# Performance work log

Measured on AMD Instinct MI355X. Metric: run time of the kernel, lower is better.

Reference implementation:

```python
import jax, jax.numpy as jnp
import numpy as np

N, E = 50000, 800000
IN, HID, OUT = 128, 32, 8


def setup_inputs() -> dict:
    key = jax.random.key(0)
    ks = jax.random.split(key, 20)
    f32 = jnp.float32
    def rn(k, shape, s=0.1):
        return (jax.random.normal(k, shape, dtype=f32) * s)
    return {
        'x': jax.random.normal(ks[0], (N, IN), dtype=f32),
        'edge_index': jax.random.randint(ks[1], (2, E), 0, N, dtype=jnp.int32),
        'edge_attr': jax.random.uniform(ks[2], (E, 1), dtype=f32),
        # layer 1: heads=4, out=HID, concat -> 4*HID channels
        'w1l': rn(ks[3], (IN, 4 * HID)), 'b1l': rn(ks[4], (4 * HID,)),
        'w1r': rn(ks[5], (IN, 4 * HID)), 'b1r': rn(ks[6], (4 * HID,)),
        'w1e': rn(ks[7], (1, 4 * HID)),
        'att1': rn(ks[8], (4, HID)), 'bias1': rn(ks[9], (4 * HID,)),
        # layer 2: heads=2, out=HID, mean over heads -> HID channels
        'w2l': rn(ks[10], (4 * HID, 2 * HID)), 'b2l': rn(ks[11], (2 * HID,)),
        'w2r': rn(ks[12], (4 * HID, 2 * HID)), 'b2r': rn(ks[13], (2 * HID,)),
        'w2e': rn(ks[14], (1, 2 * HID)),
        'att2': rn(ks[15], (2, HID)), 'bias2': rn(ks[16], (HID,)),
        'wc': rn(ks[17], (HID, OUT)), 'bc': rn(ks[18], (OUT,)),
    }


def _add_self_loops(edge_index, edge_attr, n):
    # PyG GATv2Conv adds self-loops; edge feature for loops = mean of edge_attr
    loop = jnp.arange(n, dtype=edge_index.dtype)
    src = jnp.concatenate([edge_index[0], loop])
    dst = jnp.concatenate([edge_index[1], loop])
    mean_attr = jnp.broadcast_to(edge_attr.mean(axis=0), (n, edge_attr.shape[1]))
    ea = jnp.concatenate([edge_attr, mean_attr], axis=0)
    return src, dst, ea


def _gatv2(x, src, dst, eattr, Wl, bl, Wr, br, We, att, bias, heads, out, concat):
    n = x.shape[0]
    xl = (x @ Wl + bl).reshape(n, heads, out)   # source transform (messages)
    xr = (x @ Wr + br).reshape(n, heads, out)   # target transform
    e = (eattr @ We).reshape(-1, heads, out)    # edge embedding
    z = jax.nn.leaky_relu(xl[src] + xr[dst] + e, negative_slope=0.2)  # [Etot,H,D]
    score = jnp.einsum('ehd,hd->eh', z, att)
    # segment softmax over incoming edges of each destination node
    smax = jax.ops.segment_max(score, dst, num_segments=n)
    ex = jnp.exp(score - smax[dst])
    denom = jax.ops.segment_sum(ex, dst, num_segments=n)
    alpha = ex / denom[dst]                     # [Etot,H]
    agg = jax.ops.segment_sum(xl[src] * alpha[..., None], dst, num_segments=n)
    o = agg.reshape(n, heads * out) if concat else agg.mean(axis=1)
    return o + bias


def reference(x, edge_index, edge_attr, w1l, b1l, w1r, b1r, w1e, att1, bias1,
              w2l, b2l, w2r, b2r, w2e, att2, bias2, wc, bc):
    src, dst, ea = _add_self_loops(edge_index, edge_attr, x.shape[0])
    h = _gatv2(x, src, dst, ea, w1l, b1l, w1r, b1r, w1e, att1, bias1, 4, HID, True)
    h = jax.nn.elu(h)
    # dropout p=0.4 is training-only; reference is eval mode (identity)
    h = _gatv2(h, src, dst, ea, w2l, b2l, w2r, b2r, w2e, att2, bias2, 2, HID, False)
    h = jax.nn.elu(h)
    return h @ wc + bc
```

## Files before the change

### kernel.cpp

```cpp
#include <hip/hip_runtime.h>
#include <hip/hip_fp16.h>
#include <math.h>

typedef _Float16 h2_t __attribute__((ext_vector_type(2)));
typedef _Float16 h4_t __attribute__((ext_vector_type(4)));
typedef _Float16 h8_t __attribute__((ext_vector_type(8)));
typedef float f4_t __attribute__((ext_vector_type(4)));
typedef float f8_t __attribute__((ext_vector_type(8)));

#define PRE_BLOCKS 512
#define SB 512
#define NBUK_PAD 800

__device__ inline h8_t load8f_to_h8(const float* p) {
    float4 a = *(const float4*)p;
    float4 b = *(const float4*)(p + 4);
    h8_t r;
    r[0] = (_Float16)a.x; r[1] = (_Float16)a.y; r[2] = (_Float16)a.z; r[3] = (_Float16)a.w;
    r[4] = (_Float16)b.x; r[5] = (_Float16)b.y; r[6] = (_Float16)b.z; r[7] = (_Float16)b.w;
    return r;
}

__device__ inline h4_t load4f_to_h4(const float* p) {
    float4 a = *(const float4*)p;
    h4_t r;
    r[0] = (_Float16)a.x; r[1] = (_Float16)a.y; r[2] = (_Float16)a.z; r[3] = (_Float16)a.w;
    return r;
}

__device__ inline float dot8h(h8_t a, h8_t b, float s) {
    s = __builtin_amdgcn_fdot2(__builtin_shufflevector(a, a, 0, 1),
                               __builtin_shufflevector(b, b, 0, 1), s, false);
    s = __builtin_amdgcn_fdot2(__builtin_shufflevector(a, a, 2, 3),
                               __builtin_shufflevector(b, b, 2, 3), s, false);
    s = __builtin_amdgcn_fdot2(__builtin_shufflevector(a, a, 4, 5),
                               __builtin_shufflevector(b, b, 4, 5), s, false);
    s = __builtin_amdgcn_fdot2(__builtin_shufflevector(a, a, 6, 7),
                               __builtin_shufflevector(b, b, 6, 7), s, false);
    return s;
}

__device__ inline float dot4h(h4_t a, h4_t b, float s) {
    s = __builtin_amdgcn_fdot2(__builtin_shufflevector(a, a, 0, 1),
                               __builtin_shufflevector(b, b, 0, 1), s, false);
    s = __builtin_amdgcn_fdot2(__builtin_shufflevector(a, a, 2, 3),
                               __builtin_shufflevector(b, b, 2, 3), s, false);
    return s;
}

__device__ inline float elu1(float v) { return v > 0.f ? v : __expf(v) - 1.f; }

struct MA {
    const float* x;
    const float* eattr;
    const int* ei;
    const float *w1l, *b1l, *w1r, *b1r, *w1e, *att1, *bias1;
    const float *w2l, *b2l, *w2r, *b2r, *w2e, *att2, *bias2;
    const float *wc, *bc;
    float* out;
    _Float16 *xh, *xl1h, *xr1h, *h1h, *xl2h, *xr2h;
    _Float16 *p1l, *p1r, *p2l, *p2r;
    int *deg, *offb;
    unsigned* parth;
    unsigned *tstart, *tot;
    unsigned* smeanq;
    unsigned* tmp;
    float* part;
    unsigned* edges;
    int N, E, NW, NBK, CE;
    float invE;
};


__device__ inline void phase_packw(const MA& a, int g) {
    const float* W;
    _Float16* P;
    int M, lg;
    if (g < 2048)      { W = a.w1l; P = a.p1l; M = 128; lg = g; }
    else if (g < 4096) { W = a.w1r; P = a.p1r; M = 128; lg = g - 2048; }
    else if (g < 5120) { W = a.w2l; P = a.p2l; M = 64;  lg = g - 4096; }
    else               { W = a.w2r; P = a.p2r; M = 64;  lg = g - 5120; }
    int ln = lg & 63;
    int s = (lg >> 6) & 3;
    int tt = lg >> 8;
    int m = ln & 15, quad = ln >> 4;
    h8_t v;
#pragma unroll
    for (int j = 0; j < 8; ++j)
        v[j] = (_Float16)W[(size_t)(s * 32 + quad * 8 + j) * M + tt * 16 + m];
    *(h8_t*)(P + (size_t)lg * 8) = v;
}

template <int NT>
__device__ inline void phase_mm_tile(const MA& a, const _Float16* X, int rt, int lane,
                                     const _Float16* Pl, const float* bl, _Float16* Yl,
                                     const _Float16* Pr, const float* br, _Float16* Yr) {
    int nrow = lane & 15, quad = lane >> 4;
    int row = rt * 16 + nrow;
    if (row >= a.N) return;
    const _Float16* xp = X + (size_t)row * 128 + quad * 8;
    h8_t bf0 = *(const h8_t*)(xp);
    h8_t bf1 = *(const h8_t*)(xp + 32);
    h8_t bf2 = *(const h8_t*)(xp + 64);
    h8_t bf3 = *(const h8_t*)(xp + 96);
#pragma unroll
    for (int w = 0; w < 2; ++w) {
        const _Float16* P = w ? Pr : Pl;
        const float* bias = w ? br : bl;
        _Float16* Y = w ? Yr : Yl;
#pragma unroll
        for (int t2 = 0; t2 < NT; ++t2) {
            f4_t acc = {0.f, 0.f, 0.f, 0.f};
            const _Float16* pb = P + (size_t)t2 * 2048 + (size_t)lane * 8;
            acc = __builtin_amdgcn_mfma_f32_16x16x32_f16(*(const h8_t*)pb, bf0, acc, 0, 0, 0);
            acc = __builtin_amdgcn_mfma_f32_16x16x32_f16(*(const h8_t*)(pb + 512), bf1, acc, 0, 0, 0);
            acc = __builtin_amdgcn_mfma_f32_16x16x32_f16(*(const h8_t*)(pb + 1024), bf2, acc, 0, 0, 0);
            acc = __builtin_amdgcn_mfma_f32_16x16x32_f16(*(const h8_t*)(pb + 1536), bf3, acc, 0, 0, 0);
            float4 bv = *(const float4*)(bias + t2 * 16 + quad * 4);
            h4_t o;
            o[0] = (_Float16)(acc[0] + bv.x);
            o[1] = (_Float16)(acc[1] + bv.y);
            o[2] = (_Float16)(acc[2] + bv.z);
            o[3] = (_Float16)(acc[3] + bv.w);
            *(h4_t*)(Y + (size_t)row * (NT * 16) + t2 * 16 + quad * 4) = o;
        }
    }
}


__global__ __launch_bounds__(256) void k_pre(MA a) {
    if (blockIdx.x >= PRE_BLOCKS) {
        int g = (blockIdx.x - PRE_BLOCKS) * 256 + threadIdx.x;
        if (g < 6144) phase_packw(a, g);
        return;
    }
    __shared__ unsigned bh[NBUK_PAD];
    __shared__ float sd[4];
    int tx = threadIdx.x;
    for (int j = tx; j < NBUK_PAD; j += 256) bh[j] = 0u;

    int t = blockIdx.x * 256 + tx;
    const int stride = PRE_BLOCKS * 256;
    int nchunk = (a.N * 128) >> 3;
    for (int i = t; i < nchunk; i += stride) {
        h8_t v = load8f_to_h8(a.x + (size_t)i * 8);
        *(h8_t*)(a.xh + (size_t)i * 8) = v;
    }
    float s = 0.f;
    for (int i = t; i < a.E; i += stride) s += a.eattr[i];
    for (int o = 1; o < 64; o <<= 1) s += __shfl_xor(s, o, 64);
    if ((tx & 63) == 0) sd[tx >> 6] = s;
    __syncthreads();
    if (tx == 0) a.part[blockIdx.x] = sd[0] + sd[1] + sd[2] + sd[3];

    int e0 = blockIdx.x * a.CE, e1 = min(e0 + a.CE, a.E);
    for (int e = e0 + tx; e < e1; e += 256)
        atomicAdd(&bh[((unsigned)a.ei[a.E + e]) >> 6], 1u);
    __syncthreads();
    for (int j = tx; j < NBUK_PAD; j += 256)
        a.parth[(size_t)blockIdx.x * NBUK_PAD + j] = bh[j];
}


__global__ __launch_bounds__(512, 1) void k_colscan(MA a) {
    __shared__ unsigned lds[512];
    int tx = threadIdx.x;
    int b = blockIdx.x;
    unsigned v = a.parth[(size_t)tx * NBUK_PAD + b];
    lds[tx] = v;
    __syncthreads();
    for (int o = 1; o < 512; o <<= 1) {
        unsigned u = (tx >= o) ? lds[tx - o] : 0u;
        __syncthreads();
        lds[tx] += u;
        __syncthreads();
    }
    a.parth[(size_t)tx * NBUK_PAD + b] = lds[tx] - v;
    if (tx == 511) a.tot[b] = lds[511];
}


__global__ __launch_bounds__(1024, 1) void k_scan2(MA a) {
    __shared__ unsigned lds[1024];
    __shared__ float sd[16];
    int tx = threadIdx.x;
    unsigned v = (tx < a.NBK) ? a.tot[tx] : 0u;
    lds[tx] = v;
    float s = (tx < PRE_BLOCKS) ? a.part[tx] : 0.f;
    for (int o = 1; o < 64; o <<= 1) s += __shfl_xor(s, o, 64);
    if ((tx & 63) == 0) sd[tx >> 6] = s;
    __syncthreads();
    for (int o = 1; o < 1024; o <<= 1) {
        unsigned u = (tx >= o) ? lds[tx - o] : 0u;
        __syncthreads();
        lds[tx] += u;
        __syncthreads();
    }
    if (tx < a.NBK) a.tstart[tx] = lds[tx] - v;
    if (tx == 0) {
        float m = 0.f;
#pragma unroll
        for (int k = 0; k < 16; ++k) m += sd[k];
        a.smeanq[0] = (unsigned)__float2int_rn(m * a.invE * 255.f);
    }
}


__global__ __launch_bounds__(256) void k_scatter(MA a) {
    int bid = blockIdx.x;
    if (bid < a.NW) {
        int wid = bid * 4 + (threadIdx.x >> 6);
        int ntile = (a.N + 15) / 16;
        if (wid < ntile)
            phase_mm_tile<8>(a, a.xh, wid, threadIdx.x & 63,
                             a.p1l, a.b1l, a.xl1h, a.p1r, a.b1r, a.xr1h);
        return;
    }
    __shared__ unsigned cur[NBUK_PAD];
    int s = bid - a.NW;
    int tx = threadIdx.x;
    for (int j = tx; j < NBUK_PAD; j += 256)
        cur[j] = a.parth[(size_t)s * NBUK_PAD + j] + a.tstart[j];
    __syncthreads();
    int e0 = s * a.CE, e1 = min(e0 + a.CE, a.E);
    for (int e = e0 + tx; e < e1; e += 256) {
        int d = a.ei[a.E + e];
        unsigned src = (unsigned)a.ei[e];
        unsigned q = (unsigned)__float2int_rn(a.eattr[e] * 255.f);
        unsigned pos = atomicAdd(&cur[d >> 6], 1u);
        a.tmp[pos] = src | (q << 16) | ((unsigned)(d & 63) << 24);
    }
}


__global__ __launch_bounds__(256) void k_fine(MA a) {
    __shared__ int hist[64];
    __shared__ unsigned cur[64];
    __shared__ unsigned sm;
    int b = blockIdx.x;
    int tx = threadIdx.x;
    int n0 = b << 6;
    int nn = min(64, a.N - n0);
    unsigned ts = a.tstart[b], T = a.tot[b];
    if (tx < 64) hist[tx] = 0;
    if (tx == 0) sm = a.smeanq[0];
    __syncthreads();
    for (unsigned i = tx; i < T; i += 256) {
        unsigned v = a.tmp[ts + i];
        atomicAdd(&hist[(int)(v >> 24)], 1);
    }
    __syncthreads();
    if (tx < 64) {
        int deg1 = hist[tx] + 1;
        int vsc = deg1;
#pragma unroll
        for (int o = 1; o < 64; o <<= 1) {
            int u = __shfl_up(vsc, o, 64);
            if (tx >= o) vsc += u;
        }
        int off = (int)ts + n0 + (vsc - deg1);
        if (tx < nn) {
            a.offb[n0 + tx] = off;
            a.deg[n0 + tx] = deg1;
            a.edges[off] = (unsigned)(n0 + tx) | (sm << 24);
        }
        cur[tx] = (unsigned)(off + 1);
    }
    __syncthreads();
    for (unsigned i = tx; i < T; i += 256) {
        unsigned v = a.tmp[ts + i];
        int loc = (int)(v >> 24);
        unsigned pos = atomicAdd(&cur[loc], 1u);
        a.edges[pos] = (v & 0xFFFFu) | (((v >> 16) & 0xFFu) << 24);
    }
}


__global__ __launch_bounds__(256) void k_node1(MA a) {
    int tid = threadIdx.x;
    int q = tid & 15;
    int node = blockIdx.x * 16 + (tid >> 4);
    if (node >= a.N) return;
    unsigned cb = (unsigned)(q * 16);

    h8_t xrv = *(const h8_t*)((const char*)a.xr1h + ((unsigned)node << 8) + cb);
    h8_t wev = load8f_to_h8(a.w1e + q * 8);
    h8_t atv = load8f_to_h8(a.att1 + q * 8);
    const unsigned* ep = a.edges + a.offb[node];
    int deg1 = a.deg[node];
    int last = deg1 - 1;
    const char* xb = (const char*)a.xl1h;

    float l = 0.f;
    f8_t acc = {0.f, 0.f, 0.f, 0.f, 0.f, 0.f, 0.f, 0.f};

    auto GA = [&](unsigned p) -> h8_t {
        return *(const h8_t*)(xb + (((p & 0x00FFFFFFu) << 8) | cb));
    };
    auto LOADG = [&](int i, unsigned& p0, unsigned& p1, unsigned& p2, unsigned& p3,
                     h8_t& x0, h8_t& x1, h8_t& x2, h8_t& x3) {
        p0 = ep[i];
        p1 = ep[min(i + 1, last)];
        p2 = ep[min(i + 2, last)];
        p3 = ep[min(i + 3, last)];
        x0 = GA(p0); x1 = GA(p1); x2 = GA(p2); x3 = GA(p3);
    };
    auto COMPG = [&](int i, unsigned p0, unsigned p1, unsigned p2, unsigned p3,
                     h8_t x0, h8_t x1, h8_t x2, h8_t x3) {
        float e0 = (float)(p0 >> 24) * (1.f / 255.f);
        float e1 = (float)(p1 >> 24) * (1.f / 255.f);
        float e2 = (float)(p2 >> 24) * (1.f / 255.f);
        float e3 = (float)(p3 >> 24) * (1.f / 255.f);
        h8_t z0 = x0 + xrv + wev * (_Float16)e0;
        z0 = __builtin_elementwise_max(z0, z0 * (_Float16)0.2f);
        float sc0 = dot8h(z0, atv, 0.f);
        h8_t z1 = x1 + xrv + wev * (_Float16)e1;
        z1 = __builtin_elementwise_max(z1, z1 * (_Float16)0.2f);
        float sc1 = dot8h(z1, atv, 0.f);
        h8_t z2 = x2 + xrv + wev * (_Float16)e2;
        z2 = __builtin_elementwise_max(z2, z2 * (_Float16)0.2f);
        float sc2 = dot8h(z2, atv, 0.f);
        h8_t z3 = x3 + xrv + wev * (_Float16)e3;
        z3 = __builtin_elementwise_max(z3, z3 * (_Float16)0.2f);
        float sc3 = dot8h(z3, atv, 0.f);
        sc0 += __shfl_xor(sc0, 1, 64); sc0 += __shfl_xor(sc0, 2, 64);
        sc1 += __shfl_xor(sc1, 1, 64); sc1 += __shfl_xor(sc1, 2, 64);
        sc2 += __shfl_xor(sc2, 1, 64); sc2 += __shfl_xor(sc2, 2, 64);
        sc3 += __shfl_xor(sc3, 1, 64); sc3 += __shfl_xor(sc3, 2, 64);
        float pA = __expf(fminf(sc0, 60.f));
        float pB = (i + 1 < deg1) ? __expf(fminf(sc1, 60.f)) : 0.f;
        float pC = (i + 2 < deg1) ? __expf(fminf(sc2, 60.f)) : 0.f;
        float pD = (i + 3 < deg1) ? __expf(fminf(sc3, 60.f)) : 0.f;
        l += (pA + pB) + (pC + pD);
#pragma unroll
        for (int k = 0; k < 8; ++k)
            acc[k] = fmaf(pA, (float)x0[k],
                     fmaf(pB, (float)x1[k],
                     fmaf(pC, (float)x2[k], fmaf(pD, (float)x3[k], acc[k]))));
    };

    unsigned pa0, pa1, pa2, pa3, pb0, pb1, pb2, pb3;
    h8_t xa0, xa1, xa2, xa3, xb0, xb1, xb2, xb3;
    LOADG(0, pa0, pa1, pa2, pa3, xa0, xa1, xa2, xa3);
    for (int i = 0; i < deg1; i += 8) {
        if (i + 4 < deg1) LOADG(i + 4, pb0, pb1, pb2, pb3, xb0, xb1, xb2, xb3);
        COMPG(i, pa0, pa1, pa2, pa3, xa0, xa1, xa2, xa3);
        if (i + 8 < deg1) LOADG(i + 8, pa0, pa1, pa2, pa3, xa0, xa1, xa2, xa3);
        if (i + 4 < deg1) COMPG(i + 4, pb0, pb1, pb2, pb3, xb0, xb1, xb2, xb3);
    }

    float inv = 1.f / l;
    float4 b0 = *(const float4*)(a.bias1 + q * 8);
    float4 b1 = *(const float4*)(a.bias1 + q * 8 + 4);
    float bb[8] = {b0.x, b0.y, b0.z, b0.w, b1.x, b1.y, b1.z, b1.w};
    h8_t o;
#pragma unroll
    for (int k = 0; k < 8; ++k) o[k] = (_Float16)elu1(fmaf(acc[k], inv, bb[k]));
    *(h8_t*)((char*)a.h1h + ((unsigned)node << 8) + cb) = o;
}


__global__ __launch_bounds__(256) void k_mm4(MA a) {
    int wid = blockIdx.x * 4 + (threadIdx.x >> 6);
    int ntile = (a.N + 15) / 16;
    if (wid >= ntile) return;
    phase_mm_tile<4>(a, a.h1h, wid, threadIdx.x & 63,
                     a.p2l, a.b2l, a.xl2h, a.p2r, a.b2r, a.xr2h);
}


__global__ __launch_bounds__(256) void k_node2(MA a) {
    __shared__ float h2s[16][33];
    int tid = threadIdx.x;
    int lane = tid & 63;
    int wib = tid >> 6;
    int sub = lane >> 4;
    int r = lane & 15;
    int nloc = wib * 4 + sub;
    int node = blockIdx.x * 16 + nloc;
    int c0 = r * 4;

    if (node < a.N) {
        h4_t xrv = *(const h4_t*)(a.xr2h + (size_t)node * 64 + c0);
        h4_t wev = load4f_to_h4(a.w2e + c0);
        h4_t atv = load4f_to_h4(a.att2 + c0);
        const unsigned* ep = a.edges + a.offb[node];
        int deg1 = a.deg[node];
        int last = deg1 - 1;
        const char* xb = (const char*)a.xl2h;
        unsigned cb = (unsigned)(c0 * 2);
        float l = 0.f;
        float acc[4] = {0.f, 0.f, 0.f, 0.f};
        for (int i = 0; i < deg1; i += 4) {
            unsigned p[4];
            h4_t xv[4];
#pragma unroll
            for (int j = 0; j < 4; ++j) p[j] = ep[min(i + j, last)];
#pragma unroll
            for (int j = 0; j < 4; ++j)
                xv[j] = *(const h4_t*)(xb + (((p[j] & 0x00FFFFFFu) << 7) | cb));
#pragma unroll
            for (int j = 0; j < 4; ++j) {
                float ea = (float)(p[j] >> 24) * (1.f / 255.f);
                h4_t z = xv[j] + xrv + wev * (_Float16)ea;
                z = __builtin_elementwise_max(z, z * (_Float16)0.2f);
                float sc = dot4h(z, atv, 0.f);
                sc += __shfl_xor(sc, 1, 64);
                sc += __shfl_xor(sc, 2, 64);
                sc += __shfl_xor(sc, 4, 64);
                float pp = (i + j < deg1) ? __expf(fminf(sc, 60.f)) : 0.f;
                l += pp;
#pragma unroll
                for (int k = 0; k < 4; ++k) acc[k] = fmaf(pp, (float)xv[j][k], acc[k]);
            }
        }
        float inv = 1.f / l;
#pragma unroll
        for (int k = 0; k < 4; ++k) {
            float norm = acc[k] * inv;
            float other = __shfl_xor(norm, 8, 64);
            float v = 0.5f * (norm + other);
            if (r < 8) h2s[nloc][c0 + k] = elu1(v + a.bias2[c0 + k]);
        }
    }
    __syncthreads();
    if (tid < 128) {
        int n = tid >> 3, j = tid & 7;
        int gnode = blockIdx.x * 16 + n;
        if (gnode < a.N) {
            float acc = a.bc[j];
#pragma unroll 8
            for (int d = 0; d < 32; ++d) acc = fmaf(h2s[n][d], a.wc[d * 8 + j], acc);
            a.out[(size_t)gnode * 8 + j] = acc;
        }
    }
}


extern "C" void kernel_launch(void* const* d_in, const int* in_sizes, int n_in,
                              void* d_out, int out_size, void* d_ws, size_t ws_size,
                              hipStream_t stream) {
    const int N = in_sizes[0] / 128;
    const int E = in_sizes[2];
    const int tot = E + N;

    char* ws = (char*)d_ws;
    size_t o = 0;
    auto alloc = [&](size_t bytes) -> void* {
        void* p = ws + o;
        o += (bytes + 255) & ~(size_t)255;
        return p;
    };
    MA a;
    a.x     = (const float*)d_in[0];
    a.ei    = (const int*)d_in[1];
    a.eattr = (const float*)d_in[2];
    a.w1l = (const float*)d_in[3];  a.b1l = (const float*)d_in[4];
    a.w1r = (const float*)d_in[5];  a.b1r = (const float*)d_in[6];
    a.w1e = (const float*)d_in[7];  a.att1 = (const float*)d_in[8];
    a.bias1 = (const float*)d_in[9];
    a.w2l = (const float*)d_in[10]; a.b2l = (const float*)d_in[11];
    a.w2r = (const float*)d_in[12]; a.b2r = (const float*)d_in[13];
    a.w2e = (const float*)d_in[14]; a.att2 = (const float*)d_in[15];
    a.bias2 = (const float*)d_in[16];
    a.wc = (const float*)d_in[17];  a.bc = (const float*)d_in[18];
    a.out = (float*)d_out;

    a.xh   = (_Float16*)alloc((size_t)N * 128 * 2);
    a.xl1h = (_Float16*)alloc((size_t)N * 128 * 2);
    a.xr1h = (_Float16*)alloc((size_t)N * 128 * 2);
    a.h1h  = (_Float16*)alloc((size_t)N * 128 * 2);
    a.xl2h = (_Float16*)alloc((size_t)N * 64 * 2);
    a.xr2h = (_Float16*)alloc((size_t)N * 64 * 2);
    a.p1l  = (_Float16*)alloc(128 * 128 * 2);
    a.p1r  = (_Float16*)alloc(128 * 128 * 2);
    a.p2l  = (_Float16*)alloc(128 * 64 * 2);
    a.p2r  = (_Float16*)alloc(128 * 64 * 2);
    a.deg  = (int*)alloc((size_t)N * 4);
    a.offb = (int*)alloc((size_t)N * 4);
    a.parth  = (unsigned*)alloc((size_t)SB * NBUK_PAD * 4);
    a.tstart = (unsigned*)alloc(1024 * 4);
    a.tot    = (unsigned*)alloc(1024 * 4);
    a.smeanq = (unsigned*)alloc(256);
    a.part   = (float*)alloc(PRE_BLOCKS * 4);
    a.tmp    = (unsigned*)alloc((size_t)E * 4);
    a.edges  = (unsigned*)alloc((size_t)tot * 4);
    a.N = N;
    a.E = E;
    a.NW = (N + 63) / 64;
    a.NBK = (N + 63) >> 6;
    a.CE = (E + SB - 1) / SB;
    a.invE = 1.0f / (float)E;

    k_pre<<<PRE_BLOCKS + 24, 256, 0, stream>>>(a);
    k_colscan<<<a.NBK, 512, 0, stream>>>(a);
    k_scan2<<<1, 1024, 0, stream>>>(a);
    k_scatter<<<a.NW + SB, 256, 0, stream>>>(a);
    k_fine<<<a.NBK, 256, 0, stream>>>(a);
    k_node1<<<(N + 15) / 16, 256, 0, stream>>>(a);
    k_mm4<<<(N + 63) / 64, 256, 0, stream>>>(a);
    k_node2<<<(N + 15) / 16, 256, 0, stream>>>(a);
}
```

Measured before the change: 239.3 us.

## Tile column scan over 16 buckets per block; split node1 launch in halves

The column-scan kernel now loads a 512x16 tile of per-block bucket histograms into padded shared memory and scans each column with wave-level shuffles. This replaces one block per bucket running a barrier-heavy Hillis-Steele scan, so there are far fewer blocks and barriers. Separately, the layer-1 node kernel is launched as two half-range launches using new node-range fields, which adds launch overhead with no obvious overlap benefit. The colscan grid now covers all padded buckets (800), so it also writes tot entries for padding buckets.

```diff
diff --git a/kernel.cpp b/kernel.cpp
--- a/kernel.cpp
+++ b/kernel.cpp
@@ -11,6 +11,7 @@
 #define PRE_BLOCKS 512
 #define SB 512
 #define NBUK_PAD 800
+#define CTB 16
 
 __device__ inline h8_t load8f_to_h8(const float* p) {
     float4 a = *(const float4*)p;
@@ -68,6 +69,7 @@
     float* part;
     unsigned* edges;
     int N, E, NW, NBK, CE;
+    int n0node, n1node;
     float invE;
 };
 
@@ -163,20 +165,34 @@
 
 
 __global__ __launch_bounds__(512, 1) void k_colscan(MA a) {
-    __shared__ unsigned lds[512];
+    __shared__ unsigned tile[512][CTB + 1];
     int tx = threadIdx.x;
-    int b = blockIdx.x;
-    unsigned v = a.parth[(size_t)tx * NBUK_PAD + b];
-    lds[tx] = v;
-    __syncthreads();
-    for (int o = 1; o < 512; o <<= 1) {
-        unsigned u = (tx >= o) ? lds[tx - o] : 0u;
-        __syncthreads();
-        lds[tx] += u;
-        __syncthreads();
-    }
-    a.parth[(size_t)tx * NBUK_PAD + b] = lds[tx] - v;
-    if (tx == 511) a.tot[b] = lds[511];
+    int b0 = blockIdx.x * CTB;
+    unsigned* rp = a.parth + (size_t)tx * NBUK_PAD + b0;
+#pragma unroll
+    for (int j = 0; j < CTB; ++j) tile[tx][j] = rp[j];
+    __syncthreads();
+
+    int c = tx >> 5;
+    int g = tx & 31;
+    unsigned base = 0;
+#pragma unroll
+    for (int k = 0; k < 16; ++k) {
+        int r = k * 32 + g;
+        unsigned orig = tile[r][c];
+        unsigned v = orig;
+#pragma unroll
+        for (int o = 1; o < 32; o <<= 1) {
+            unsigned u = __shfl_up(v, o, 32);
+            if (g >= o) v += u;
+        }
+        tile[r][c] = base + (v - orig);
+        base += __shfl(v, 31, 32);
+    }
+    if (g == 0) a.tot[b0 + c] = base;
+    __syncthreads();
+#pragma unroll
+    for (int j = 0; j < CTB; ++j) rp[j] = tile[tx][j];
 }
 
 
@@ -279,8 +295,8 @@
 __global__ __launch_bounds__(256) void k_node1(MA a) {
     int tid = threadIdx.x;
     int q = tid & 15;
-    int node = blockIdx.x * 16 + (tid >> 4);
-    if (node >= a.N) return;
+    int node = a.n0node + blockIdx.x * 16 + (tid >> 4);
+    if (node >= a.n1node) return;
     unsigned cb = (unsigned)(q * 16);
 
     h8_t xrv = *(const h8_t*)((const char*)a.xr1h + ((unsigned)node << 8) + cb);
@@ -493,11 +509,17 @@
     a.invE = 1.0f / (float)E;
 
     k_pre<<<PRE_BLOCKS + 24, 256, 0, stream>>>(a);
-    k_colscan<<<a.NBK, 512, 0, stream>>>(a);
+    k_colscan<<<NBUK_PAD / CTB, 512, 0, stream>>>(a);
     k_scan2<<<1, 1024, 0, stream>>>(a);
     k_scatter<<<a.NW + SB, 256, 0, stream>>>(a);
     k_fine<<<a.NBK, 256, 0, stream>>>(a);
-    k_node1<<<(N + 15) / 16, 256, 0, stream>>>(a);
+
+    int mid = ((N / 2) + 15) & ~15;
+    MA a1 = a; a1.n0node = 0;   a1.n1node = mid;
+    MA a2 = a; a2.n0node = mid; a2.n1node = N;
+    k_node1<<<mid / 16, 256, 0, stream>>>(a1);
+    k_node1<<<(N - mid + 15) / 16, 256, 0, stream>>>(a2);
+
     k_mm4<<<(N + 63) / 64, 256, 0, stream>>>(a);
     k_node2<<<(N + 15) / 16, 256, 0, stream>>>(a);
 }
```

New measurement: 247.5 us. 1.03x slower.
